# Optimization experiments

Measured on AMD Instinct MI355X. Metric: run time of the kernel, lower is better.

The kernel has to match this reference:

```python
import jax, jax.numpy as jnp
import numpy as np

B, T, U, V = 8, 256, 64, 1024


def setup_inputs() -> dict:
    key = jax.random.key(0)
    k1, k2, k3, k4, k5, k6 = jax.random.split(key, 6)
    logits = jax.random.normal(k1, (B, T, U, V), dtype=jnp.float32)
    # soft labels are a probability distribution over vocab per (b, u)
    soft_labels = jax.nn.softmax(jax.random.normal(k2, (B, U, V), dtype=jnp.float32), axis=-1)
    # monotonic alignment: time index per label position, in [0, T)
    aligns = jnp.sort(jax.random.randint(k3, (B, U), 0, T, dtype=jnp.int32), axis=-1)
    xlens = jax.random.randint(k4, (B,), T // 2, T + 1, dtype=jnp.int32)
    ylens = jax.random.randint(k5, (B,), 1, U + 1, dtype=jnp.int32)  # >= 1
    ys = jax.random.randint(k6, (B, U), 0, V, dtype=jnp.int32)  # unused by the loss, kept for signature parity
    return {"logits": logits, "ys": ys, "soft_labels": soft_labels,
            "aligns": aligns, "xlens": xlens, "ylens": ylens}


def reference(logits, ys, soft_labels, aligns, xlens, ylens):
    # Faithful to the torch code: the inner `for u` loop overwrites loss_u,
    # so only u = ylen-1 survives for each batch element.
    bs = logits.shape[0]
    b = jnp.arange(bs)
    u_last = ylens - 1                           # [B]
    t_last = aligns[b, u_last]                   # [B], time index at last label
    sel = logits[b, t_last, u_last]              # [B, V]
    logp = jax.nn.log_softmax(sel, axis=-1)      # [B, V]
    loss_u = jnp.sum(soft_labels[b, u_last] * logp, axis=-1)  # [B]
    loss_u = loss_u / ylens.astype(logits.dtype)  # normalize_length=True
    loss = -jnp.sum(loss_u)
    return loss / bs                              # normalize_batch=True
```

## Files before the change

kernel.cpp:

```cpp
#include <hip/hip_runtime.h>

#define BB 8
#define TT 256
#define UU 64
#define VV 1024

__global__ __launch_bounds__(256) void rnnt_align_distill_loss_kernel(
    const float* __restrict__ logits,
    const float* __restrict__ soft_labels,
    const int*   __restrict__ aligns,
    const int*   __restrict__ ylens,
    float* __restrict__ out)
{
    const int tid  = threadIdx.x;
    const int lane = tid & 63;
    const int wave = tid >> 6;

    __shared__ float red_m[4];
    __shared__ float red_se[4];
    __shared__ float red_dot[4];
    __shared__ float red_sp[4];

    float total = 0.0f;

    for (int b = 0; b < BB; ++b) {
        const int ylen = ylens[b];
        const int u    = ylen - 1;
        const int t    = aligns[b * UU + u];

        const float* sel = logits + ((((size_t)b * TT + t) * UU + u) * VV);
        const float* sp  = soft_labels + (((size_t)b * UU + u) * VV);

        float x[4], p[4];
        #pragma unroll
        for (int i = 0; i < 4; ++i) {
            const int v = tid + i * 256;
            x[i] = sel[v];
            p[i] = sp[v];
        }

        float m = fmaxf(fmaxf(x[0], x[1]), fmaxf(x[2], x[3]));
        #pragma unroll
        for (int off = 32; off > 0; off >>= 1)
            m = fmaxf(m, __shfl_down(m, off, 64));
        if (lane == 0) red_m[wave] = m;
        __syncthreads();
        m = fmaxf(fmaxf(red_m[0], red_m[1]), fmaxf(red_m[2], red_m[3]));
        __syncthreads();

        float se = 0.0f, dot = 0.0f, sump = 0.0f;
        #pragma unroll
        for (int i = 0; i < 4; ++i) {
            se   += expf(x[i] - m);
            dot  += p[i] * x[i];
            sump += p[i];
        }
        #pragma unroll
        for (int off = 32; off > 0; off >>= 1) {
            se   += __shfl_down(se,   off, 64);
            dot  += __shfl_down(dot,  off, 64);
            sump += __shfl_down(sump, off, 64);
        }
        if (lane == 0) { red_se[wave] = se; red_dot[wave] = dot; red_sp[wave] = sump; }
        __syncthreads();

        if (tid == 0) {
            const float se_t   = red_se[0] + red_se[1] + red_se[2] + red_se[3];
            const float dot_t  = red_dot[0] + red_dot[1] + red_dot[2] + red_dot[3];
            const float sump_t = red_sp[0] + red_sp[1] + red_sp[2] + red_sp[3];
            const float lse    = m + logf(se_t);
            const float loss_u = (dot_t - lse * sump_t) / (float)ylen;
            total += loss_u;
        }
        __syncthreads();
    }

    if (tid == 0) {
        out[0] = -total / (float)BB;
    }
}

extern "C" void kernel_launch(void* const* d_in, const int* in_sizes, int n_in,
                              void* d_out, int out_size, void* d_ws, size_t ws_size,
                              hipStream_t stream) {
    const float* logits      = (const float*)d_in[0];
    const float* soft_labels = (const float*)d_in[2];
    const int*   aligns      = (const int*)d_in[3];
    const int*   ylens       = (const int*)d_in[5];
    float* out = (float*)d_out;

    rnnt_align_distill_loss_kernel<<<1, 256, 0, stream>>>(
        logits, soft_labels, aligns, ylens, out);
}
```

Measured before the change: 586.5 us.

## Process all batch rows in parallel with one wavefront per row

```diff
diff --git a/kernel.cpp b/kernel.cpp
--- a/kernel.cpp
+++ b/kernel.cpp
@@ -5,7 +5,7 @@
 #define UU 64
 #define VV 1024
 
-__global__ __launch_bounds__(256) void rnnt_align_distill_loss_kernel(
+__global__ __launch_bounds__(512) void rnnt_align_distill_loss_kernel(
     const float* __restrict__ logits,
     const float* __restrict__ soft_labels,
     const int*   __restrict__ aligns,
@@ -14,68 +14,57 @@
 {
     const int tid  = threadIdx.x;
     const int lane = tid & 63;
-    const int wave = tid >> 6;
+    const int b    = tid >> 6;
 
-    __shared__ float red_m[4];
-    __shared__ float red_se[4];
-    __shared__ float red_dot[4];
-    __shared__ float red_sp[4];
+    __shared__ float red_loss[BB];
 
-    float total = 0.0f;
+    const int ylen = ylens[b];
+    const int u    = ylen - 1;
+    const int t    = aligns[b * UU + u];
 
-    for (int b = 0; b < BB; ++b) {
-        const int ylen = ylens[b];
-        const int u    = ylen - 1;
-        const int t    = aligns[b * UU + u];
+    const float* sel = logits + ((((size_t)b * TT + t) * UU + u) * VV);
+    const float* sp  = soft_labels + (((size_t)b * UU + u) * VV);
 
-        const float* sel = logits + ((((size_t)b * TT + t) * UU + u) * VV);
-        const float* sp  = soft_labels + (((size_t)b * UU + u) * VV);
-
-        float x[4], p[4];
-        #pragma unroll
-        for (int i = 0; i < 4; ++i) {
-            const int v = tid + i * 256;
-            x[i] = sel[v];
-            p[i] = sp[v];
-        }
-
-        float m = fmaxf(fmaxf(x[0], x[1]), fmaxf(x[2], x[3]));
-        #pragma unroll
-        for (int off = 32; off > 0; off >>= 1)
-            m = fmaxf(m, __shfl_down(m, off, 64));
-        if (lane == 0) red_m[wave] = m;
-        __syncthreads();
-        m = fmaxf(fmaxf(red_m[0], red_m[1]), fmaxf(red_m[2], red_m[3]));
-        __syncthreads();
-
-        float se = 0.0f, dot = 0.0f, sump = 0.0f;
-        #pragma unroll
-        for (int i = 0; i < 4; ++i) {
-            se   += expf(x[i] - m);
-            dot  += p[i] * x[i];
-            sump += p[i];
-        }
-        #pragma unroll
-        for (int off = 32; off > 0; off >>= 1) {
-            se   += __shfl_down(se,   off, 64);
-            dot  += __shfl_down(dot,  off, 64);
-            sump += __shfl_down(sump, off, 64);
-        }
-        if (lane == 0) { red_se[wave] = se; red_dot[wave] = dot; red_sp[wave] = sump; }
-        __syncthreads();
-
-        if (tid == 0) {
-            const float se_t   = red_se[0] + red_se[1] + red_se[2] + red_se[3];
-            const float dot_t  = red_dot[0] + red_dot[1] + red_dot[2] + red_dot[3];
-            const float sump_t = red_sp[0] + red_sp[1] + red_sp[2] + red_sp[3];
-            const float lse    = m + logf(se_t);
-            const float loss_u = (dot_t - lse * sump_t) / (float)ylen;
-            total += loss_u;
-        }
-        __syncthreads();
+    float x[16], p[16];
+    #pragma unroll
+    for (int i = 0; i < 16; ++i) {
+        const int v = lane + i * 64;
+        x[i] = sel[v];
+        p[i] = sp[v];
     }
 
+    float m = x[0];
+    #pragma unroll
+    for (int i = 1; i < 16; ++i) m = fmaxf(m, x[i]);
+    #pragma unroll
+    for (int off = 32; off > 0; off >>= 1)
+        m = fmaxf(m, __shfl_down(m, off, 64));
+    m = __shfl(m, 0, 64);
+
+    float se = 0.0f, dot = 0.0f, sump = 0.0f;
+    #pragma unroll
+    for (int i = 0; i < 16; ++i) {
+        se   += expf(x[i] - m);
+        dot  += p[i] * x[i];
+        sump += p[i];
+    }
+    #pragma unroll
+    for (int off = 32; off > 0; off >>= 1) {
+        se   += __shfl_down(se,   off, 64);
+        dot  += __shfl_down(dot,  off, 64);
+        sump += __shfl_down(sump, off, 64);
+    }
+
+    if (lane == 0) {
+        const float lse    = m + logf(se);
+        red_loss[b] = (dot - lse * sump) / (float)ylen;
+    }
+    __syncthreads();
+
     if (tid == 0) {
+        float total = 0.0f;
+        #pragma unroll
+        for (int i = 0; i < BB; ++i) total += red_loss[i];
         out[0] = -total / (float)BB;
     }
 }
@@ -89,6 +78,6 @@
     const int*   ylens       = (const int*)d_in[5];
     float* out = (float*)d_out;
 
-    rnnt_align_distill_loss_kernel<<<1, 256, 0, stream>>>(
+    rnnt_align_distill_loss_kernel<<<1, 512, 0, stream>>>(
         logits, soft_labels, aligns, ylens, out);
 }
```

After: 567.2 us. 3.3% less time.
